# Kernel optimization log

Measured on AMD Instinct MI355X. Metric: run time of the kernel, lower is better.

Reference implementation:

```python
import jax, jax.numpy as jnp
import numpy as np
from jax import lax

B, C, H, W = 4, 3, 512, 512
PATCH = 64
STRIDE = 32
CHANS = [(3, 32), (32, 32), (32, 64), (64, 64), (64, 64), (64, 32), (32, 32), (32, 2)]


def _conv(x, w, b):
    y = lax.conv_general_dilated(x, w, (1, 1), [(1, 1), (1, 1)],
                                 dimension_numbers=('NCHW', 'OIHW', 'NCHW'))
    return y + b[None, :, None, None]


def _pool(x):  # MaxPool2d(2)
    return lax.reduce_window(x, -jnp.inf, lax.max, (1, 1, 2, 2), (1, 1, 2, 2), 'VALID')


def _up(x):  # Upsample(scale=2, bilinear, align_corners=False) == half-pixel resize
    b, c, h, w = x.shape
    return jax.image.resize(x, (b, c, 2 * h, 2 * w), 'bilinear')


def _flow_net(x, ws, bs):
    r = jax.nn.relu
    h = r(_conv(x, ws[0], bs[0]))
    h = r(_conv(h, ws[1], bs[1]))
    h = _pool(h)
    h = r(_conv(h, ws[2], bs[2]))
    h = r(_conv(h, ws[3], bs[3]))
    h = _pool(h)
    h = _up(h)
    h = r(_conv(h, ws[4], bs[4]))
    h = r(_conv(h, ws[5], bs[5]))
    h = _up(h)
    h = r(_conv(h, ws[6], bs[6]))
    return jnp.tanh(_conv(h, ws[7], bs[7]))  # [B,2,H,W]


def _bilinear_zeros(img, gx, gy):
    # img [C,H,W], gx/gy [N,P,P] in [-1,1]; grid_sample bilinear, zeros padding, align_corners=False
    Hh, Ww = img.shape[1], img.shape[2]
    ix = ((gx + 1.0) * Ww - 1.0) * 0.5
    iy = ((gy + 1.0) * Hh - 1.0) * 0.5
    x0 = jnp.floor(ix)
    y0 = jnp.floor(iy)
    wx1 = ix - x0
    wy1 = iy - y0

    def corner(xi, yi, wgt):
        valid = (xi >= 0) & (xi <= Ww - 1) & (yi >= 0) & (yi <= Hh - 1)
        xc = jnp.clip(xi, 0, Ww - 1).astype(jnp.int32)
        yc = jnp.clip(yi, 0, Hh - 1).astype(jnp.int32)
        return img[:, yc, xc] * (wgt * valid)[None]  # [C,N,P,P]

    return (corner(x0, y0, (1 - wx1) * (1 - wy1))
            + corner(x0 + 1, y0, wx1 * (1 - wy1))
            + corner(x0, y0 + 1, (1 - wx1) * wy1)
            + corner(x0 + 1, y0 + 1, wx1 * wy1))


def _forward(x, ws, bs, temp):
    b, c, h, w = x.shape
    flow = _flow_net(x, ws, bs)  # [B,2,H,W]
    gy, gx = jnp.meshgrid(jnp.linspace(-1.0, 1.0, h), jnp.linspace(-1.0, 1.0, w), indexing='ij')
    base = jnp.stack([gx, gy], axis=-1)  # [H,W,2] (x,y)
    deformed = base[None] + flow.transpose(0, 2, 3, 1) * temp  # [B,H,W,2]
    centers = deformed[:, ::STRIDE, ::STRIDE, :].reshape(b, -1, 2)  # [B,N,2]
    py, px = jnp.meshgrid(jnp.linspace(-1.0, 1.0, PATCH), jnp.linspace(-1.0, 1.0, PATCH), indexing='ij')
    pgx = centers[:, :, None, None, 0] + px[None, None] * (PATCH / w)  # [B,N,P,P]
    pgy = centers[:, :, None, None, 1] + py[None, None] * (PATCH / h)
    patches = jax.vmap(_bilinear_zeros)(x, pgx, pgy)  # [B,C,N,P,P]
    patches = patches.transpose(0, 2, 1, 3, 4)  # [B,N,C,P,P]
    return patches, flow, deformed


def setup_inputs() -> dict:
    key = jax.random.key(0)
    ks = jax.random.split(key, len(CHANS) + 1)
    d = {"x": jax.random.normal(ks[0], (B, C, H, W), jnp.float32)}
    for i, (ci, co) in enumerate(CHANS):
        d[f"w{i}"] = jax.random.normal(ks[i + 1], (co, ci, 3, 3), jnp.float32) * 0.01
        d[f"b{i}"] = jnp.zeros((co,), jnp.float32)
    d["temp"] = jnp.full((1,), 0.1, jnp.float32)
    return d


def reference(x, w0, b0, w1, b1, w2, b2, w3, b3, w4, b4, w5, b5, w6, b6, w7, b7, temp):
    ws = [w0, w1, w2, w3, w4, w5, w6, w7]
    bs = [b0, b1, b2, b3, b4, b5, b6, b7]
    return _forward(x, ws, bs, temp)
```

## Files before the change

### kernel.cpp

```cpp
#include <hip/hip_runtime.h>
#include <hip/hip_bf16.h>

typedef __hip_bfloat16 bf16;
typedef unsigned short ushort_t;
typedef __attribute__((ext_vector_type(8))) short short8;
typedef __attribute__((ext_vector_type(4))) float float4v;

#define BATCH 4
#define HH 512
#define WW 512

#define WO_L0 0
#define WO_L1 3072
#define WO_L2 12288
#define WO_L3 30720
#define WO_L4P 67584
#define WO_L5 215040
#define WO_L6P 233472
#define WO_L7 270336
#define WO_L4U 274944
#define WO_L6U 311808

__device__ __forceinline__ ushort_t f2bfu(float f) {
  __hip_bfloat16 h = __float2bfloat16(f);
// ... 24 lines not shown
  const int job = blockIdx.y;
  const int e = blockIdx.x * 256 + threadIdx.x;
  if (job == 0) {
    if (e >= 3072) return;
    int c = e & 7;
    int o = (e >> 3) & 31;
    int g = (e >> 8) % 3;
    int tl = (e >> 8) / 3;
    int tap = g * 4 + tl;
    float v = 0.0f;
    if (tap < 9 && c < 3) v = wp.w[0][(o * 3 + c) * 9 + tap];
    dst[WO_L0 + e] = __float2bfloat16(v);
    return;
  }
  if (job == 4 || job == 6) {
    const int O = (job == 4) ? 64 : 32;
    const int I = O;
    const int NCH = I >> 5;
    const int n = 4 * NCH * 9 * O * 32;
    if (e >= n) return;
    int ic = e & 31;
    int o = (e >> 5) % O;
    int tap = (e / (32 * O)) % 9;
    int ch = (e / (9 * 32 * O)) % NCH;
    int ph = e / (NCH * 9 * 32 * O);
    int i = ch * 32 + ic;
    int u = tap / 3, v2 = tap - u * 3;
    int dy = ph >> 1, dx = ph & 1;
    const float* w = wp.w[job];
    float acc = 0.0f;
#pragma unroll
    for (int r = 0; r < 3; ++r) {
      float ry = upw(r + dy, u);
#pragma unroll
      for (int s = 0; s < 3; ++s)
        acc += w[(o * I + i) * 9 + r * 3 + s] * ry * upw(s + dx, v2);
    }
    dst[((job == 4) ? WO_L4P : WO_L6P) + e] = __float2bfloat16(acc);
    return;
  }
  int O, I, OP, off;
  const float* w;
  if (job == 1)      { O = 32; I = 32; OP = 32; off = WO_L1; w = wp.w[1]; }
  else if (job == 2) { O = 64; I = 32; OP = 64; off = WO_L2; w = wp.w[2]; }
  else if (job == 3) { O = 64; I = 64; OP = 64; off = WO_L3; w = wp.w[3]; }
  else if (job == 5) { O = 32; I = 64; OP = 32; off = WO_L5; w = wp.w[5]; }
  else if (job == 7) { O = 2;  I = 32; OP = 16; off = WO_L7; w = wp.w[7]; }
  else if (job == 8) { O = 64; I = 64; OP = 64; off = WO_L4U; w = wp.w[4]; }
  else               { O = 32; I = 32; OP = 32; off = WO_L6U; w = wp.w[6]; }
  const int NCH = I >> 5;
  const int n = NCH * 9 * OP * 32;
  if (e >= n) return;
  int ic = e & 31;
  int o = (e >> 5) % OP;
  int tap = (e / (32 * OP)) % 9;
  int ch = e / (9 * 32 * OP);
  int i = ch * 32 + ic;
  float v = 0.0f;
  if (o < O) v = w[(o * I + i) * 9 + tap];
  dst[off + e] = __float2bfloat16(v);
}

__global__ __launch_bounds__(256) void pack_x(const float* __restrict__ x,
                                              bf16* __restrict__ xp) {
  int i = blockIdx.x * 256 + threadIdx.x;
  if (i >= BATCH * HH * WW) return;
  int b = i / (HH * WW);
  int px = i - b * (HH * WW);
  union { uint4 v; ushort_t s[8]; } o;
  o.v = make_uint4(0, 0, 0, 0);
  const float* p = x + (long)b * 3 * HH * WW + px;
  o.s[0] = f2bfu(p[0]);
  o.s[1] = f2bfu(p[HH * WW]);
  o.s[2] = f2bfu(p[2 * HH * WW]);
  *(uint4*)&xp[(long)i * 8] = o.v;
}

__global__ __launch_bounds__(512) void conv01_k(
    const bf16* __restrict__ xp, const bf16* __restrict__ w0,
    const bf16* __restrict__ w1, const float* __restrict__ b0,
    const float* __restrict__ b1, bf16* __restrict__ out) {
  __shared__ alignas(16) bf16 xp_lds[720 * 8];
  __shared__ alignas(16) bf16 mid_lds[612 * 32];
  __shared__ alignas(16) bf16 w0_lds[3072];
  __shared__ alignas(16) bf16 w1_lds[9 * 32 * 32];
  const int tid = threadIdx.x;
  const int lane = tid & 63;
  const int wid = tid >> 6;
  const int lm = lane & 15;
  const int quad = lane >> 4;
  const int x0 = blockIdx.x * 16, y0 = blockIdx.y * 32;
  const int b = blockIdx.z;

  for (int u = tid; u < 720; u += 512) {
    int hy = u / 20, hx = u - hy * 20;
    int gy = y0 - 2 + hy, gx = x0 - 2 + hx;
    uint4 v = make_uint4(0, 0, 0, 0);
    if (gy >= 0 && gy < HH && gx >= 0 && gx < WW)
      v = *(const uint4*)(xp + (((long)b * HH + gy) * WW + gx) * 8);
    *(uint4*)&xp_lds[u * 8] = v;
  }
  if (tid < 384) *(uint4*)&w0_lds[tid * 8] = *(const uint4*)(w0 + tid * 8);
  for (int j = wid; j < 18; j += 8)
    dma16((char*)w1_lds + j * 1024, (const char*)w1 + j * 1024 + lane * 16);
  __syncthreads();

  for (int t = wid; t < 39; t += 8) {
    int px = t * 16 + lm;
    int pxc = min(px, 611);
    int hy = pxc / 18, hx = pxc - hy * 18;
    float4v acc0[2];
#pragma unroll
    for (int mt = 0; mt < 2; ++mt)
      acc0[mt] = *(const float4v*)(b0 + mt * 16 + quad * 4);
#pragma unroll
    for (int g = 0; g < 3; ++g) {
      int tap = g * 4 + quad;
      if (tap > 8) tap = 8;
      int r = (tap * 11) >> 5;
      int s = tap - r * 3;
      short8 bfr = *(const short8*)&xp_lds[((hy + r) * 20 + hx + s) * 8];
      short8 a0 = *(const short8*)&w0_lds[quad * 768 + (g * 32 + lm) * 8];
      short8 a1 = *(const short8*)&w0_lds[quad * 768 + (g * 32 + 16 + lm) * 8];
      acc0[0] = __builtin_amdgcn_mfma_f32_16x16x32_bf16(a0, bfr, acc0[0], 0, 0, 0);
      acc0[1] = __builtin_amdgcn_mfma_f32_16x16x32_bf16(a1, bfr, acc0[1], 0, 0, 0);
    }
    int gy = y0 - 1 + hy, gx = x0 - 1 + hx;
    bool inimg = (gy >= 0) && (gy < HH) && (gx >= 0) && (gx < WW);
    if (px < 612) {
#pragma unroll
      for (int mt = 0; mt < 2; ++mt) {
        union { uint2 v; ushort_t s2[4]; } pk;
#pragma unroll
        for (int r2 = 0; r2 < 4; ++r2)
          pk.s2[r2] = inimg ? f2bfu(fmaxf(acc0[mt][r2], 0.0f)) : (ushort_t)0;
        *(uint2*)&mid_lds[px * 32 + mt * 16 + quad * 4] = pk.v;
      }
    }
  }
  __syncthreads();

  float4v acc[2][4];
#pragma unroll
  for (int mt = 0; mt < 2; ++mt) {
    float4v bv = *(const float4v*)(b1 + mt * 16 + quad * 4);
#pragma unroll
    for (int nt = 0; nt < 4; ++nt) acc[mt][nt] = bv;
  }
#pragma unroll
  for (int tap = 0; tap < 9; ++tap) {
    const int r = tap / 3, s = tap - r * 3;
    short8 afrag[2], bfrag[4];
#pragma unroll
    for (int mt = 0; mt < 2; ++mt)
      afrag[mt] = *(const short8*)&w1_lds[(tap * 32 + mt * 16 + lm) * 32 + quad * 8];
#pragma unroll
    for (int nt = 0; nt < 4; ++nt) {
      int py = 4 * wid + nt;
      bfrag[nt] = *(const short8*)&mid_lds[((py + r) * 18 + lm + s) * 32 + quad * 8];
    }
#pragma unroll
    for (int mt = 0; mt < 2; ++mt)
#pragma unroll
      for (int nt = 0; nt < 4; ++nt)
        acc[mt][nt] = __builtin_amdgcn_mfma_f32_16x16x32_bf16(
            afrag[mt], bfrag[nt], acc[mt][nt], 0, 0, 0);
  }
  const int Ho = HH >> 1, Wo = WW >> 1;
#pragma unroll
  for (int mt = 0; mt < 2; ++mt) {
#pragma unroll
    for (int g = 0; g < 2; ++g) {
      float4v m;
#pragma unroll
      for (int r = 0; r < 4; ++r)
        m[r] = fmaxf(fmaxf(acc[mt][2 * g][r], acc[mt][2 * g + 1][r]), 0.0f);
#pragma unroll
      for (int r = 0; r < 4; ++r) m[r] = fmaxf(m[r], __shfl_xor(m[r], 1, 64));
      if ((lm & 1) == 0) {
        int pyo = (y0 >> 1) + 2 * wid + g;
        int pxo = (x0 >> 1) + (lm >> 1);
        union { uint2 v; ushort_t s[4]; } pk;
#pragma unroll
        for (int r = 0; r < 4; ++r) pk.s[r] = f2bfu(m[r]);
        *(uint2*)&out[(((long)b * Ho + pyo) * Wo + pxo) * 32 + mt * 16 +
                      quad * 4] = pk.v;
      }
    }
  }
}

template <int CIN, int COUT, int COUTR, int OUT_MODE>
__global__ __launch_bounds__(512) void conv_mfma(
    const bf16* __restrict__ in, const bf16* __restrict__ wt,
    const float* __restrict__ bias, void* __restrict__ out_, int H, int W,
    const float* __restrict__ temp, float* __restrict__ def) {
  constexpr int MT = COUT / 16;
  constexpr int CK = 32;
  __shared__ alignas(16) bf16 in_lds[612 * CK];
  __shared__ alignas(16) bf16 w_lds[9 * COUT * CK];
  const int tid = threadIdx.x;
  const int lane = tid & 63;
  const int wid = tid >> 6;
  const int lm = lane & 15;
  const int quad = lane >> 4;
  const int x0 = blockIdx.x * 16;
  const int y0 = blockIdx.y * 32;
  const int b = blockIdx.z;

  float4v acc[MT][4];
#pragma unroll
  for (int mt = 0; mt < MT; ++mt) {
    float4v bv;
    if constexpr (COUTR == COUT) {
      bv = *(const float4v*)(bias + mt * 16 + quad * 4);
    } else {
#pragma unroll
      for (int r = 0; r < 4; ++r) {
        int co = mt * 16 + quad * 4 + r;
        bv[r] = (co < COUTR) ? bias[co] : 0.0f;
      }
    }
#pragma unroll
    for (int nt = 0; nt < 4; ++nt) acc[mt][nt] = bv;
  }

  const bool interior =
      (x0 >= 1) && (x0 + 16 <= W - 1) && (y0 >= 1) && (y0 + 32 <= H - 1);
  for (int c0 = 0; c0 < CIN; c0 += CK) {
    if (interior) {
      for (int r = wid; r < 34; r += 8) {
        int gy = y0 - 1 + r;
        const bf16* gsrc = in + (((long)b * H + gy) * W + x0) * CIN + c0 +
                           (lane >> 2) * CIN + (lane & 3) * 8;
        dma16(&in_lds[(r * 18 + 1) * CK], gsrc);
      }
      if (tid < 272) {
        int r = tid >> 3;
        int side = (tid >> 2) & 1;
        int seg = tid & 3;
        int gx = side ? (x0 + 16) : (x0 - 1);
        int gy = y0 - 1 + r;
        uint4 v = *(const uint4*)(in + (((long)b * H + gy) * W + gx) * CIN +
                                  c0 + seg * 8);
        *(uint4*)&in_lds[(r * 18 + (side ? 17 : 0)) * CK + seg * 8] = v;
      }
    } else {
      for (int u = tid; u < 612 * 4; u += 512) {
        int px = u >> 2;
        int seg = u & 3;
        int hy = px / 18, hx = px - hy * 18;
        int gy = y0 - 1 + hy, gx = x0 - 1 + hx;
        uint4 v = make_uint4(0, 0, 0, 0);
        if (gy >= 0 && gy < H && gx >= 0 && gx < W)
          v = *(const uint4*)(in + (((long)b * H + gy) * W + gx) * CIN + c0 +
                              seg * 8);
        *(uint4*)&in_lds[px * CK + seg * 8] = v;
      }
    }
    {
      const char* wsrc = (const char*)(wt + (size_t)(c0 >> 5) * 9 * COUT * CK);
      constexpr int WCH = 9 * COUT * CK * 2 / 1024;
      for (int j = wid; j < WCH; j += 8)
        dma16((char*)w_lds + j * 1024, wsrc + j * 1024 + lane * 16);
    }
    __syncthreads();

#pragma unroll
    for (int tap = 0; tap < 9; ++tap) {
      const int r = tap / 3, s = tap - r * 3;
      short8 afrag[MT], bfrag[4];
#pragma unroll
      for (int mt = 0; mt < MT; ++mt)
        afrag[mt] =
            *(const short8*)&w_lds[(tap * COUT + mt * 16 + lm) * CK + quad * 8];
#pragma unroll
      for (int nt = 0; nt < 4; ++nt) {
        int py = 4 * wid + nt;
        bfrag[nt] =
            *(const short8*)&in_lds[((py + r) * 18 + lm + s) * CK + quad * 8];
      }
#pragma unroll
      for (int mt = 0; mt < MT; ++mt)
#pragma unroll
        for (int nt = 0; nt < 4; ++nt)
          acc[mt][nt] = __builtin_amdgcn_mfma_f32_16x16x32_bf16(
              afrag[mt], bfrag[nt], acc[mt][nt], 0, 0, 0);
    }
    __syncthreads();
  }

  if constexpr (OUT_MODE == 3) {
    bf16* out = (bf16*)out_;
    const int Ho = H >> 1, Wo = W >> 1;
#pragma unroll
    for (int mt = 0; mt < MT; ++mt) {
#pragma unroll
      for (int g = 0; g < 2; ++g) {
        float4v m;
#pragma unroll
        for (int r = 0; r < 4; ++r)
          m[r] = fmaxf(fmaxf(acc[mt][2 * g][r], acc[mt][2 * g + 1][r]), 0.0f);
#pragma unroll
        for (int r = 0; r < 4; ++r) m[r] = fmaxf(m[r], __shfl_xor(m[r], 1, 64));
        if ((lm & 1) == 0) {
          int pyo = (y0 >> 1) + 2 * wid + g;
          int pxo = (x0 >> 1) + (lm >> 1);
          union { uint2 v; ushort_t s[4]; } pk;
#pragma unroll
          for (int r = 0; r < 4; ++r) pk.s[r] = f2bfu(m[r]);
          *(uint2*)&out[(((long)b * Ho + pyo) * Wo + pxo) * COUT + mt * 16 +
                        quad * 4] = pk.v;
        }
      }
    }
  } else {
#pragma unroll
    for (int mt = 0; mt < MT; ++mt) {
#pragma unroll
      for (int nt = 0; nt < 4; ++nt) {
        int gy = y0 + 4 * wid + nt;
        int gx = x0 + lm;
        float4v v = acc[mt][nt];
        if constexpr (OUT_MODE == 0) {
          bf16* out = (bf16*)out_;
          union { uint2 v; ushort_t s[4]; } pk;
#pragma unroll
          for (int r = 0; r < 4; ++r) pk.s[r] = f2bfu(fmaxf(v[r], 0.0f));
          *(uint2*)&out[(((long)b * H + gy) * W + gx) * COUT + mt * 16 +
                        quad * 4] = pk.v;
        } else {
          float* out = (float*)out_;
          if (quad == 0) {
            float fx = tanhf(v[0]);
            float fy = tanhf(v[1]);
            out[(((long)b * 2 + 0) * H + gy) * (long)W + gx] = fx;
            out[(((long)b * 2 + 1) * H + gy) * (long)W + gx] = fy;
            float T = temp[0];
            float2 d;
            d.x = -1.0f + gx * (2.0f / 511.0f) + fx * T;
            d.y = -1.0f + gy * (2.0f / 511.0f) + fy * T;
            *(float2*)&def[(((long)b * HH + gy) * WW + gx) * 2] = d;
          }
        }
      }
    }
  }
}

template <int CIN, int COUT, bool PSPLIT>
__global__ __launch_bounds__(512) void conv_up(
    const bf16* __restrict__ in, const bf16* __restrict__ wtP,
    const bf16* __restrict__ wtU, const float* __restrict__ bias,
    bf16* __restrict__ out, int Ho, int Wo) {
  constexpr int MT = COUT / 16;
  constexpr int MH = MT / 2;
  constexpr int CK = 32;
  constexpr int WSZ = 9 * COUT * CK;
  constexpr int WBUF = PSPLIT ? WSZ : 2 * WSZ;
  __shared__ alignas(16) bf16 in_lds[612 * CK];
  __shared__ alignas(16) bf16 w_lds[WBUF];
  const int tid = threadIdx.x;
  const int lane = tid & 63;
  const int wid = tid >> 6;
  const int lm = lane & 15;
  const int quad = lane >> 4;
  const int Hs = Ho >> 1, Ws = Wo >> 1;
  const int nx = Ws >> 4, ny = Hs >> 5;
  const int bulkN = nx * ny;
  const int b = PSPLIT ? (blockIdx.z >> 2) : blockIdx.z;
  const int ph0 = PSPLIT ? (blockIdx.z & 3) : 0;
  const int t = blockIdx.x;

  if (t >= bulkN) {
    if (PSPLIT && ph0 != 0) return;
    const int G = Wo >> 4;
    int e = t - bulkN;
    int tx, ty;
    if (e < G) { ty = 0; tx = e; }
    else if (e < 2 * G) { ty = G - 1; tx = e - G; }
    else { int u = e - 2 * G; ty = 1 + (u >> 1); tx = (u & 1) ? (G - 1) : 0; }
    const int x0 = tx * 16, y0 = ty * 16;
    const int wrow = wid & 3;
    const int wmt = (wid >> 2) * MH;

    float4v acc[MH][4];
#pragma unroll
    for (int m = 0; m < MH; ++m) {
      float4v bv = *(const float4v*)(bias + (wmt + m) * 16 + quad * 4);
#pragma unroll
      for (int nt = 0; nt < 4; ++nt) acc[m][nt] = bv;
    }

    for (int c0 = 0; c0 < CIN; c0 += CK) {
      for (int u = tid; u < 324 * 4; u += 512) {
        int px = u >> 2;
        int seg = u & 3;
        int hy = px / 18, hx = px - hy * 18;
        int gy = y0 - 1 + hy, gx = x0 - 1 + hx;
        uint4 o = make_uint4(0, 0, 0, 0);
        if (gy >= 0 && gy < Ho && gx >= 0 && gx < Wo) {
          int ys = (gy >> 1) - ((gy & 1) ? 0 : 1);
          int xs = (gx >> 1) - ((gx & 1) ? 0 : 1);
          float wy = (gy & 1) ? 0.25f : 0.75f;
          float wx = (gx & 1) ? 0.25f : 0.75f;
          int y0c = max(ys, 0), y1c = min(ys + 1, Hs - 1);
          int x0c = max(xs, 0), x1c = min(xs + 1, Ws - 1);
          const bf16* p = in + ((long)b * Hs * Ws) * CIN + c0 + seg * 8;
          union { uint4 v; ushort_t s[8]; } a00, a01, a10, a11, r;
          a00.v = *(const uint4*)(p + ((long)y0c * Ws + x0c) * CIN);
          a01.v = *(const uint4*)(p + ((long)y0c * Ws + x1c) * CIN);
          a10.v = *(const uint4*)(p + ((long)y1c * Ws + x0c) * CIN);
          a11.v = *(const uint4*)(p + ((long)y1c * Ws + x1c) * CIN);
#pragma unroll
          for (int j = 0; j < 8; ++j) {
            float f = (1.0f - wy) * ((1.0f - wx) * bfu2f(a00.s[j]) +
                                     wx * bfu2f(a01.s[j])) +
                      wy * ((1.0f - wx) * bfu2f(a10.s[j]) +
                            wx * bfu2f(a11.s[j]));
            r.s[j] = f2bfu(f);
          }
          o = r.v;
        }
        *(uint4*)&in_lds[px * CK + seg * 8] = o;
      }
      {
        const char* wsrc = (const char*)(wtU + (size_t)(c0 >> 5) * WSZ);
        constexpr int WCH = WSZ * 2 / 1024;
        for (int j = wid; j < WCH; j += 8)
          dma16((char*)w_lds + j * 1024, wsrc + j * 1024 + lane * 16);
      }
      __syncthreads();
#pragma unroll
      for (int tap = 0; tap < 9; ++tap) {
        const int r = tap / 3, s = tap - r * 3;
        short8 afrag[MH], bfrag[4];
#pragma unroll
        for (int m = 0; m < MH; ++m)
          afrag[m] = *(const short8*)&w_lds[(tap * COUT + (wmt + m) * 16 + lm) * CK +
                                            quad * 8];
#pragma unroll
        for (int nt = 0; nt < 4; ++nt) {
          int py = 4 * wrow + nt;
          bfrag[nt] =
              *(const short8*)&in_lds[((py + r) * 18 + lm + s) * CK + quad * 8];
        }
#pragma unroll
        for (int m = 0; m < MH; ++m)
#pragma unroll
          for (int nt = 0; nt < 4; ++nt)
            acc[m][nt] = __builtin_amdgcn_mfma_f32_16x16x32_bf16(
                afrag[m], bfrag[nt], acc[m][nt], 0, 0, 0);
      }
      __syncthreads();
    }
#pragma unroll
    for (int m = 0; m < MH; ++m)
#pragma unroll
      for (int nt = 0; nt < 4; ++nt) {
        int gy = y0 + 4 * wrow + nt;
        int gx = x0 + lm;
        union { uint2 v; ushort_t s[4]; } pk;
#pragma unroll
        for (int r = 0; r < 4; ++r) pk.s[r] = f2bfu(fmaxf(acc[m][nt][r], 0.0f));
        *(uint2*)&out[(((long)b * Ho + gy) * Wo + gx) * COUT + (wmt + m) * 16 +
                      quad * 4] = pk.v;
      }
    return;
  }

  const int bx = t % nx, by = t / nx;
  const int xs0 = bx * 16, ys0 = by * 32;
  const bool interior = (bx >= 1) && (bx < nx - 1) && (by >= 1) && (by < ny - 1);

  if constexpr (!PSPLIT) {
    static_assert(CIN == CK, "non-split bulk path assumes single K chunk");
    if (interior) {
      for (int r = wid; r < 34; r += 8) {
        int gy = ys0 - 1 + r;
        const bf16* gsrc = in + (((long)b * Hs + gy) * Ws + xs0) * CIN +
                           (lane >> 2) * CIN + (lane & 3) * 8;
        dma16(&in_lds[(r * 18 + 1) * CK], gsrc);
      }
      if (tid < 272) {
        int r = tid >> 3;
        int side = (tid >> 2) & 1;
        int seg = tid & 3;
        int gx = side ? (xs0 + 16) : (xs0 - 1);
        int gy = ys0 - 1 + r;
        uint4 v = *(const uint4*)(in + (((long)b * Hs + gy) * Ws + gx) * CIN +
                                  seg * 8);
        *(uint4*)&in_lds[(r * 18 + (side ? 17 : 0)) * CK + seg * 8] = v;
      }
    } else {
      for (int u = tid; u < 612 * 4; u += 512) {
        int px = u >> 2;
        int seg = u & 3;
        int hy = px / 18, hx = px - hy * 18;
        int sy = min(max(ys0 - 1 + hy, 0), Hs - 1);
        int sx = min(max(xs0 - 1 + hx, 0), Ws - 1);
        uint4 v = *(const uint4*)(in + (((long)b * Hs + sy) * Ws + sx) * CIN +
                                  seg * 8);
        *(uint4*)&in_lds[px * CK + seg * 8] = v;
      }
    }
    constexpr int WCH = 2 * WSZ * 2 / 1024;
    for (int pair = 0; pair < 2; ++pair) {
      {
        const char* wsrc = (const char*)(wtP + (size_t)(2 * pair) * WSZ);
        for (int j = wid; j < WCH; j += 8)
          dma16((char*)w_lds + j * 1024, wsrc + j * 1024 + lane * 16);
      }
      __syncthreads();
      float4v acc[2][MT][4];
#pragma unroll
      for (int p = 0; p < 2; ++p)
#pragma unroll
        for (int mt = 0; mt < MT; ++mt) {
          float4v bv = *(const float4v*)(bias + mt * 16 + quad * 4);
#pragma unroll
          for (int nt = 0; nt < 4; ++nt) acc[p][mt][nt] = bv;
        }
#pragma unroll
      for (int tap = 0; tap < 9; ++tap) {
        const int r = tap / 3, s = tap - r * 3;
        short8 bfrag[4], afrag[2][MT];
#pragma unroll
        for (int nt = 0; nt < 4; ++nt) {
          int py = 4 * wid + nt;
          bfrag[nt] =
              *(const short8*)&in_lds[((py + r) * 18 + lm + s) * CK + quad * 8];
        }
#pragma unroll
        for (int p = 0; p < 2; ++p)
#pragma unroll
          for (int mt = 0; mt < MT; ++mt)
            afrag[p][mt] = *(const short8*)&w_lds[p * WSZ +
                (tap * COUT + mt * 16 + lm) * CK + quad * 8];
#pragma unroll
        for (int p = 0; p < 2; ++p)
#pragma unroll
          for (int mt = 0; mt < MT; ++mt)
#pragma unroll
            for (int nt = 0; nt < 4; ++nt)
              acc[p][mt][nt] = __builtin_amdgcn_mfma_f32_16x16x32_bf16(
                  afrag[p][mt], bfrag[nt], acc[p][mt][nt], 0, 0, 0);
      }
      const int dy = pair;
#pragma unroll
      for (int p = 0; p < 2; ++p) {
        const int dx = p;
#pragma unroll
        for (int mt = 0; mt < MT; ++mt)
#pragma unroll
          for (int nt = 0; nt < 4; ++nt) {
            int gy = 2 * (ys0 + 4 * wid + nt) + dy;
            int gx = 2 * (xs0 + lm) + dx;
            if (gy >= 16 && gy < Ho - 16 && gx >= 16 && gx < Wo - 16) {
              union { uint2 v; ushort_t s2[4]; } pk;
#pragma unroll
              for (int r2 = 0; r2 < 4; ++r2)
                pk.s2[r2] = f2bfu(fmaxf(acc[p][mt][nt][r2], 0.0f));
              *(uint2*)&out[(((long)b * Ho + gy) * Wo + gx) * COUT + mt * 16 +
                            quad * 4] = pk.v;
            }
          }
      }
      __syncthreads();
    }
    return;
  }

  const int ph = ph0;
  float4v acc[MT][4];
#pragma unroll
  for (int mt = 0; mt < MT; ++mt) {
    float4v bv = *(const float4v*)(bias + mt * 16 + quad * 4);
#pragma unroll
    for (int nt = 0; nt < 4; ++nt) acc[mt][nt] = bv;
  }
  for (int c0 = 0; c0 < CIN; c0 += CK) {
    if (interior) {
      for (int r = wid; r < 34; r += 8) {
        int gy = ys0 - 1 + r;
        const bf16* gsrc = in + (((long)b * Hs + gy) * Ws + xs0) * CIN +
                           c0 + (lane >> 2) * CIN + (lane & 3) * 8;
        dma16(&in_lds[(r * 18 + 1) * CK], gsrc);
      }
      if (tid < 272) {
        int r = tid >> 3;
        int side = (tid >> 2) & 1;
        int seg = tid & 3;
        int gx = side ? (xs0 + 16) : (xs0 - 1);
        int gy = ys0 - 1 + r;
        uint4 v = *(const uint4*)(in + (((long)b * Hs + gy) * Ws + gx) * CIN +
                                  c0 + seg * 8);
        *(uint4*)&in_lds[(r * 18 + (side ? 17 : 0)) * CK + seg * 8] = v;
      }
    } else {
      for (int u = tid; u < 612 * 4; u += 512) {
        int px = u >> 2;
        int seg = u & 3;
        int hy = px / 18, hx = px - hy * 18;
        int sy = min(max(ys0 - 1 + hy, 0), Hs - 1);
        int sx = min(max(xs0 - 1 + hx, 0), Ws - 1);
        uint4 v = *(const uint4*)(in + (((long)b * Hs + sy) * Ws + sx) * CIN +
                                  seg * 8);
        *(uint4*)&in_lds[px * CK + seg * 8] = v;
      }
    }
    {
      const char* wsrc = (const char*)(wtP + (size_t)(ph * (CIN / CK) + (c0 >> 5)) * WSZ);
      constexpr int WCH = WSZ * 2 / 1024;
      for (int j = wid; j < WCH; j += 8)
        dma16((char*)w_lds + j * 1024, wsrc + j * 1024 + lane * 16);
    }
    __syncthreads();
#pragma unroll
    for (int tap = 0; tap < 9; ++tap) {
      const int r = tap / 3, s = tap - r * 3;
      short8 afrag[MT], bfrag[4];
#pragma unroll
      for (int mt = 0; mt < MT; ++mt)
        afrag[mt] =
            *(const short8*)&w_lds[(tap * COUT + mt * 16 + lm) * CK + quad * 8];
#pragma unroll
      for (int nt = 0; nt < 4; ++nt) {
        int py = 4 * wid + nt;
        bfrag[nt] =
            *(const short8*)&in_lds[((py + r) * 18 + lm + s) * CK + quad * 8];
      }
#pragma unroll
      for (int mt = 0; mt < MT; ++mt)
#pragma unroll
        for (int nt = 0; nt < 4; ++nt)
          acc[mt][nt] = __builtin_amdgcn_mfma_f32_16x16x32_bf16(
              afrag[mt], bfrag[nt], acc[mt][nt], 0, 0, 0);
    }
    __syncthreads();
  }
  const int dy = ph >> 1, dx = ph & 1;
#pragma unroll
  for (int mt = 0; mt < MT; ++mt)
#pragma unroll
    for (int nt = 0; nt < 4; ++nt) {
      int gy = 2 * (ys0 + 4 * wid + nt) + dy;
      int gx = 2 * (xs0 + lm) + dx;
      if (gy >= 16 && gy < Ho - 16 && gx >= 16 && gx < Wo - 16) {
        union { uint2 v; ushort_t s2[4]; } pk;
#pragma unroll
        for (int r2 = 0; r2 < 4; ++r2)
          pk.s2[r2] = f2bfu(fmaxf(acc[mt][nt][r2], 0.0f));
        *(uint2*)&out[(((long)b * Ho + gy) * Wo + gx) * COUT + mt * 16 +
                      quad * 4] = pk.v;
      }
    }
}

__global__ __launch_bounds__(256) void patches_k(const float* __restrict__ x,
                                                 const float* __restrict__ def,
                                                 float* __restrict__ out) {
  int i = blockIdx.x * 256 + threadIdx.x;
  int pj = i & 63;
  int t = i >> 6;
  int pi = t & 63;
  t >>= 6;
  int n = t & 255;
  int b = t >> 8;
  if (b >= BATCH) return;
  int hi = n >> 4, wi = n & 15;
  const float* dptr = def + (((long)b * HH + hi * 32) * WW + wi * 32) * 2;
  float cx = dptr[0], cy = dptr[1];
  float pgx = cx + (-1.0f + pj * (2.0f / 63.0f)) * 0.125f;
  float pgy = cy + (-1.0f + pi * (2.0f / 63.0f)) * 0.125f;
  float ix = ((pgx + 1.0f) * 512.0f - 1.0f) * 0.5f;
  float iy = ((pgy + 1.0f) * 512.0f - 1.0f) * 0.5f;
  float fx0 = floorf(ix), fy0 = floorf(iy);
  float wx1 = ix - fx0, wy1 = iy - fy0;
  int x0 = (int)fx0, y0 = (int)fy0;
  int x1 = x0 + 1, y1 = y0 + 1;
  bool vx0 = (x0 >= 0) && (x0 <= 511), vx1 = (x1 >= 0) && (x1 <= 511);
  bool vy0 = (y0 >= 0) && (y0 <= 511), vy1 = (y1 >= 0) && (y1 <= 511);
  int cx0 = min(max(x0, 0), 511), cx1 = min(max(x1, 0), 511);
  int cy0 = min(max(y0, 0), 511), cy1 = min(max(y1, 0), 511);
  float w00 = (1.0f - wx1) * (1.0f - wy1) * ((vx0 && vy0) ? 1.0f : 0.0f);
  float w01 = wx1 * (1.0f - wy1) * ((vx1 && vy0) ? 1.0f : 0.0f);
  float w10 = (1.0f - wx1) * wy1 * ((vx0 && vy1) ? 1.0f : 0.0f);
  float w11 = wx1 * wy1 * ((vx1 && vy1) ? 1.0f : 0.0f);
#pragma unroll
  for (int c = 0; c < 3; ++c) {
    const float* img = x + ((long)b * 3 + c) * (HH * WW);
    float v = img[cy0 * WW + cx0] * w00 + img[cy0 * WW + cx1] * w01 +
              img[cy1 * WW + cx0] * w10 + img[cy1 * WW + cx1] * w11;
    out[(((long)b * 256 + n) * 3 + c) * 4096 + pi * 64 + pj] = v;
  }
}


extern "C" void kernel_launch(void* const* d_in, const int* in_sizes, int n_in,
                              void* d_out, int out_size, void* d_ws,
                              size_t ws_size, hipStream_t stream) {
  const float* x = (const float*)d_in[0];
  WP wp;
  const float* bs[8];
  for (int i = 0; i < 8; ++i) {
    wp.w[i] = (const float*)d_in[1 + 2 * i];
    bs[i] = (const float*)d_in[2 + 2 * i];
  }
  const float* temp = (const float*)d_in[17];

  float* out = (float*)d_out;
  float* flow = out + 12582912;
  float* def = out + 14680064;
  bf16* wT = (bf16*)d_out;

  const size_t bufElems = (size_t)BATCH * 512 * 512 * 32;
  bf16* A = (bf16*)d_ws;
  bf16* Bf = A + bufElems;
  bf16* xp = Bf + bufElems;

  prep_w<<<dim3(576, 10), 256, 0, stream>>>(wp, wT);
  pack_x<<<(BATCH * HH * WW) / 256, 256, 0, stream>>>(x, xp);
// ... 18 lines not shown
```

Baseline: 317.5 us.

## Read conv weight fragments directly from global memory instead of staging in LDS

Removes the LDS weight buffers from all conv kernels and loads the MFMA A-fragments straight from global memory, relying on L1/L2 caching of the small weight tensors. This drops the per-chunk weight DMA and cuts LDS usage, which may allow more blocks per CU, and it reorders barriers so only one sync sits between chunk iterations. The cost is more global and cache traffic inside the MFMA inner loop, which adds latency there. It also fixes a missing c0 offset in the edge-tile load path of the upsampled conv.

```diff
diff --git a/kernel.cpp b/kernel.cpp
--- a/kernel.cpp
+++ b/kernel.cpp
@@ -130,8 +130,6 @@
     const float* __restrict__ b1, bf16* __restrict__ out) {
   __shared__ alignas(16) bf16 xp_lds[720 * 8];
   __shared__ alignas(16) bf16 mid_lds[612 * 32];
-  __shared__ alignas(16) bf16 w0_lds[3072];
-  __shared__ alignas(16) bf16 w1_lds[9 * 32 * 32];
   const int tid = threadIdx.x;
   const int lane = tid & 63;
   const int wid = tid >> 6;
@@ -148,9 +146,6 @@
       v = *(const uint4*)(xp + (((long)b * HH + gy) * WW + gx) * 8);
     *(uint4*)&xp_lds[u * 8] = v;
   }
-  if (tid < 384) *(uint4*)&w0_lds[tid * 8] = *(const uint4*)(w0 + tid * 8);
-  for (int j = wid; j < 18; j += 8)
-    dma16((char*)w1_lds + j * 1024, (const char*)w1 + j * 1024 + lane * 16);
   __syncthreads();
 
   for (int t = wid; t < 39; t += 8) {
@@ -168,8 +163,8 @@
       int r = (tap * 11) >> 5;
       int s = tap - r * 3;
       short8 bfr = *(const short8*)&xp_lds[((hy + r) * 20 + hx + s) * 8];
-      short8 a0 = *(const short8*)&w0_lds[quad * 768 + (g * 32 + lm) * 8];
-      short8 a1 = *(const short8*)&w0_lds[quad * 768 + (g * 32 + 16 + lm) * 8];
+      short8 a0 = *(const short8*)&w0[quad * 768 + (g * 32 + lm) * 8];
+      short8 a1 = *(const short8*)&w0[quad * 768 + (g * 32 + 16 + lm) * 8];
       acc0[0] = __builtin_amdgcn_mfma_f32_16x16x32_bf16(a0, bfr, acc0[0], 0, 0, 0);
       acc0[1] = __builtin_amdgcn_mfma_f32_16x16x32_bf16(a1, bfr, acc0[1], 0, 0, 0);
     }
@@ -201,7 +196,7 @@
     short8 afrag[2], bfrag[4];
 #pragma unroll
     for (int mt = 0; mt < 2; ++mt)
-      afrag[mt] = *(const short8*)&w1_lds[(tap * 32 + mt * 16 + lm) * 32 + quad * 8];
+      afrag[mt] = *(const short8*)&w1[(tap * 32 + mt * 16 + lm) * 32 + quad * 8];
 #pragma unroll
     for (int nt = 0; nt < 4; ++nt) {
       int py = 4 * wid + nt;
@@ -246,7 +241,6 @@
   constexpr int MT = COUT / 16;
   constexpr int CK = 32;
   __shared__ alignas(16) bf16 in_lds[612 * CK];
-  __shared__ alignas(16) bf16 w_lds[9 * COUT * CK];
   const int tid = threadIdx.x;
   const int lane = tid & 63;
   const int wid = tid >> 6;
@@ -276,6 +270,7 @@
   const bool interior =
       (x0 >= 1) && (x0 + 16 <= W - 1) && (y0 >= 1) && (y0 + 32 <= H - 1);
   for (int c0 = 0; c0 < CIN; c0 += CK) {
+    if (c0) __syncthreads();
     if (interior) {
       for (int r = wid; r < 34; r += 8) {
         int gy = y0 - 1 + r;
@@ -306,14 +301,9 @@
         *(uint4*)&in_lds[px * CK + seg * 8] = v;
       }
     }
-    {
-      const char* wsrc = (const char*)(wt + (size_t)(c0 >> 5) * 9 * COUT * CK);
-      constexpr int WCH = 9 * COUT * CK * 2 / 1024;
-      for (int j = wid; j < WCH; j += 8)
-        dma16((char*)w_lds + j * 1024, wsrc + j * 1024 + lane * 16);
-    }
     __syncthreads();
 
+    const bf16* wc = wt + (size_t)(c0 >> 5) * 9 * COUT * CK;
 #pragma unroll
     for (int tap = 0; tap < 9; ++tap) {
       const int r = tap / 3, s = tap - r * 3;
@@ -321,7 +311,7 @@
 #pragma unroll
       for (int mt = 0; mt < MT; ++mt)
         afrag[mt] =
-            *(const short8*)&w_lds[(tap * COUT + mt * 16 + lm) * CK + quad * 8];
+            *(const short8*)&wc[(tap * COUT + mt * 16 + lm) * CK + quad * 8];
 #pragma unroll
       for (int nt = 0; nt < 4; ++nt) {
         int py = 4 * wid + nt;
@@ -335,7 +325,6 @@
           acc[mt][nt] = __builtin_amdgcn_mfma_f32_16x16x32_bf16(
               afrag[mt], bfrag[nt], acc[mt][nt], 0, 0, 0);
     }
-    __syncthreads();
   }
 
   if constexpr (OUT_MODE == 3) {
@@ -405,9 +394,7 @@
   constexpr int MH = MT / 2;
   constexpr int CK = 32;
   constexpr int WSZ = 9 * COUT * CK;
-  constexpr int WBUF = PSPLIT ? WSZ : 2 * WSZ;
   __shared__ alignas(16) bf16 in_lds[612 * CK];
-  __shared__ alignas(16) bf16 w_lds[WBUF];
   const int tid = threadIdx.x;
   const int lane = tid & 63;
   const int wid = tid >> 6;
@@ -441,6 +428,7 @@
     }
 
     for (int c0 = 0; c0 < CIN; c0 += CK) {
+      if (c0) __syncthreads();
       for (int u = tid; u < 324 * 4; u += 512) {
         int px = u >> 2;
         int seg = u & 3;
@@ -472,21 +460,16 @@
         }
         *(uint4*)&in_lds[px * CK + seg * 8] = o;
       }
-      {
-        const char* wsrc = (const char*)(wtU + (size_t)(c0 >> 5) * WSZ);
-        constexpr int WCH = WSZ * 2 / 1024;
-        for (int j = wid; j < WCH; j += 8)
-          dma16((char*)w_lds + j * 1024, wsrc + j * 1024 + lane * 16);
-      }
       __syncthreads();
+      const bf16* wc = wtU + (size_t)(c0 >> 5) * WSZ;
 #pragma unroll
       for (int tap = 0; tap < 9; ++tap) {
         const int r = tap / 3, s = tap - r * 3;
         short8 afrag[MH], bfrag[4];
 #pragma unroll
         for (int m = 0; m < MH; ++m)
-          afrag[m] = *(const short8*)&w_lds[(tap * COUT + (wmt + m) * 16 + lm) * CK +
-                                            quad * 8];
+          afrag[m] = *(const short8*)&wc[(tap * COUT + (wmt + m) * 16 + lm) * CK +
+                                         quad * 8];
 #pragma unroll
         for (int nt = 0; nt < 4; ++nt) {
           int py = 4 * wrow + nt;
@@ -500,7 +483,6 @@
             acc[m][nt] = __builtin_amdgcn_mfma_f32_16x16x32_bf16(
                 afrag[m], bfrag[nt], acc[m][nt], 0, 0, 0);
       }
-      __syncthreads();
     }
 #pragma unroll
     for (int m = 0; m < MH; ++m)
@@ -552,14 +534,9 @@
         *(uint4*)&in_lds[px * CK + seg * 8] = v;
       }
     }
-    constexpr int WCH = 2 * WSZ * 2 / 1024;
+    __syncthreads();
+
     for (int pair = 0; pair < 2; ++pair) {
-      {
-        const char* wsrc = (const char*)(wtP + (size_t)(2 * pair) * WSZ);
-        for (int j = wid; j < WCH; j += 8)
-          dma16((char*)w_lds + j * 1024, wsrc + j * 1024 + lane * 16);
-      }
-      __syncthreads();
       float4v acc[2][MT][4];
 #pragma unroll
       for (int p = 0; p < 2; ++p)
@@ -569,6 +546,7 @@
 #pragma unroll
           for (int nt = 0; nt < 4; ++nt) acc[p][mt][nt] = bv;
         }
+      const bf16* w0p = wtP + (size_t)(2 * pair) * WSZ;
 #pragma unroll
       for (int tap = 0; tap < 9; ++tap) {
         const int r = tap / 3, s = tap - r * 3;
@@ -583,7 +561,7 @@
         for (int p = 0; p < 2; ++p)
 #pragma unroll
           for (int mt = 0; mt < MT; ++mt)
-            afrag[p][mt] = *(const short8*)&w_lds[p * WSZ +
+            afrag[p][mt] = *(const short8*)&w0p[(size_t)p * WSZ +
                 (tap * COUT + mt * 16 + lm) * CK + quad * 8];
 #pragma unroll
         for (int p = 0; p < 2; ++p)
@@ -614,7 +592,6 @@
             }
           }
       }
-      __syncthreads();
     }
     return;
   }
@@ -628,6 +605,7 @@
     for (int nt = 0; nt < 4; ++nt) acc[mt][nt] = bv;
   }
   for (int c0 = 0; c0 < CIN; c0 += CK) {
+    if (c0) __syncthreads();
     if (interior) {
       for (int r = wid; r < 34; r += 8) {
         int gy = ys0 - 1 + r;
@@ -653,17 +631,12 @@
         int sy = min(max(ys0 - 1 + hy, 0), Hs - 1);
         int sx = min(max(xs0 - 1 + hx, 0), Ws - 1);
         uint4 v = *(const uint4*)(in + (((long)b * Hs + sy) * Ws + sx) * CIN +
-                                  seg * 8);
+                                  c0 + seg * 8);
         *(uint4*)&in_lds[px * CK + seg * 8] = v;
       }
     }
-    {
-      const char* wsrc = (const char*)(wtP + (size_t)(ph * (CIN / CK) + (c0 >> 5)) * WSZ);
-      constexpr int WCH = WSZ * 2 / 1024;
-      for (int j = wid; j < WCH; j += 8)
-        dma16((char*)w_lds + j * 1024, wsrc + j * 1024 + lane * 16);
-    }
     __syncthreads();
+    const bf16* wc = wtP + (size_t)(ph * (CIN / CK) + (c0 >> 5)) * WSZ;
 #pragma unroll
     for (int tap = 0; tap < 9; ++tap) {
       const int r = tap / 3, s = tap - r * 3;
@@ -671,7 +644,7 @@
 #pragma unroll
       for (int mt = 0; mt < MT; ++mt)
         afrag[mt] =
-            *(const short8*)&w_lds[(tap * COUT + mt * 16 + lm) * CK + quad * 8];
+            *(const short8*)&wc[(tap * COUT + mt * 16 + lm) * CK + quad * 8];
 #pragma unroll
       for (int nt = 0; nt < 4; ++nt) {
         int py = 4 * wid + nt;
@@ -685,7 +658,6 @@
           acc[mt][nt] = __builtin_amdgcn_mfma_f32_16x16x32_bf16(
               afrag[mt], bfrag[nt], acc[mt][nt], 0, 0, 0);
     }
-    __syncthreads();
   }
   const int dy = ph >> 1, dx = ph & 1;
 #pragma unroll
```

New measurement: 359.6 us. +13.3%, slower.

## Stage conv weights in LDS one kernel row at a time to cut LDS footprint

Applied to the files above, without the earlier changes.

The weight tile in shared memory now holds only 3 taps (one kernel row) instead of all 9, in both conv_mfma and conv_up. Each input-channel chunk now runs three load/sync/compute rounds that reuse the same input halo. The aim is to free LDS so more blocks fit on each CU. The cost is three times as many barriers and weight loads that are exposed rather than overlapped. The clamped border path of the phase-split branch also now adds the missing c0 channel offset, which fixes a correctness bug when CIN is greater than 32.

```diff
diff --git a/kernel.cpp b/kernel.cpp
--- a/kernel.cpp
+++ b/kernel.cpp
@@ -246,7 +246,7 @@
   constexpr int MT = COUT / 16;
   constexpr int CK = 32;
   __shared__ alignas(16) bf16 in_lds[612 * CK];
-  __shared__ alignas(16) bf16 w_lds[9 * COUT * CK];
+  __shared__ alignas(16) bf16 w_lds[3 * COUT * CK];
   const int tid = threadIdx.x;
   const int lane = tid & 63;
   const int wid = tid >> 6;
@@ -276,66 +276,71 @@
   const bool interior =
       (x0 >= 1) && (x0 + 16 <= W - 1) && (y0 >= 1) && (y0 + 32 <= H - 1);
   for (int c0 = 0; c0 < CIN; c0 += CK) {
-    if (interior) {
-      for (int r = wid; r < 34; r += 8) {
-        int gy = y0 - 1 + r;
-        const bf16* gsrc = in + (((long)b * H + gy) * W + x0) * CIN + c0 +
-                           (lane >> 2) * CIN + (lane & 3) * 8;
-        dma16(&in_lds[(r * 18 + 1) * CK], gsrc);
-      }
-      if (tid < 272) {
-        int r = tid >> 3;
-        int side = (tid >> 2) & 1;
-        int seg = tid & 3;
-        int gx = side ? (x0 + 16) : (x0 - 1);
-        int gy = y0 - 1 + r;
-        uint4 v = *(const uint4*)(in + (((long)b * H + gy) * W + gx) * CIN +
+    for (int tg = 0; tg < 3; ++tg) {
+      if (tg == 0) {
+        if (interior) {
+          for (int r = wid; r < 34; r += 8) {
+            int gy = y0 - 1 + r;
+            const bf16* gsrc = in + (((long)b * H + gy) * W + x0) * CIN + c0 +
+                               (lane >> 2) * CIN + (lane & 3) * 8;
+            dma16(&in_lds[(r * 18 + 1) * CK], gsrc);
+          }
+          if (tid < 272) {
+            int r = tid >> 3;
+            int side = (tid >> 2) & 1;
+            int seg = tid & 3;
+            int gx = side ? (x0 + 16) : (x0 - 1);
+            int gy = y0 - 1 + r;
+            uint4 v = *(const uint4*)(in + (((long)b * H + gy) * W + gx) * CIN +
+                                      c0 + seg * 8);
+            *(uint4*)&in_lds[(r * 18 + (side ? 17 : 0)) * CK + seg * 8] = v;
+          }
+        } else {
+          for (int u = tid; u < 612 * 4; u += 512) {
+            int px = u >> 2;
+            int seg = u & 3;
+            int hy = px / 18, hx = px - hy * 18;
+            int gy = y0 - 1 + hy, gx = x0 - 1 + hx;
+            uint4 v = make_uint4(0, 0, 0, 0);
+            if (gy >= 0 && gy < H && gx >= 0 && gx < W)
+              v = *(const uint4*)(in + (((long)b * H + gy) * W + gx) * CIN +
                                   c0 + seg * 8);
-        *(uint4*)&in_lds[(r * 18 + (side ? 17 : 0)) * CK + seg * 8] = v;
-      }
-    } else {
-      for (int u = tid; u < 612 * 4; u += 512) {
-        int px = u >> 2;
-        int seg = u & 3;
-        int hy = px / 18, hx = px - hy * 18;
-        int gy = y0 - 1 + hy, gx = x0 - 1 + hx;
-        uint4 v = make_uint4(0, 0, 0, 0);
-        if (gy >= 0 && gy < H && gx >= 0 && gx < W)
-          v = *(const uint4*)(in + (((long)b * H + gy) * W + gx) * CIN + c0 +
-                              seg * 8);
-        *(uint4*)&in_lds[px * CK + seg * 8] = v;
-      }
-    }
-    {
-      const char* wsrc = (const char*)(wt + (size_t)(c0 >> 5) * 9 * COUT * CK);
-      constexpr int WCH = 9 * COUT * CK * 2 / 1024;
-      for (int j = wid; j < WCH; j += 8)
-        dma16((char*)w_lds + j * 1024, wsrc + j * 1024 + lane * 16);
-    }
-    __syncthreads();
-
-#pragma unroll
-    for (int tap = 0; tap < 9; ++tap) {
-      const int r = tap / 3, s = tap - r * 3;
-      short8 afrag[MT], bfrag[4];
-#pragma unroll
-      for (int mt = 0; mt < MT; ++mt)
-        afrag[mt] =
-            *(const short8*)&w_lds[(tap * COUT + mt * 16 + lm) * CK + quad * 8];
-#pragma unroll
-      for (int nt = 0; nt < 4; ++nt) {
-        int py = 4 * wid + nt;
-        bfrag[nt] =
-            *(const short8*)&in_lds[((py + r) * 18 + lm + s) * CK + quad * 8];
-      }
-#pragma unroll
-      for (int mt = 0; mt < MT; ++mt)
-#pragma unroll
-        for (int nt = 0; nt < 4; ++nt)
-          acc[mt][nt] = __builtin_amdgcn_mfma_f32_16x16x32_bf16(
-              afrag[mt], bfrag[nt], acc[mt][nt], 0, 0, 0);
-    }
-    __syncthreads();
+            *(uint4*)&in_lds[px * CK + seg * 8] = v;
+          }
+        }
+      }
+      {
+        const char* wsrc =
+            (const char*)(wt + ((size_t)(c0 >> 5) * 9 + 3 * tg) * COUT * CK);
+        constexpr int WCH = 3 * COUT * CK * 2 / 1024;
+        for (int j = wid; j < WCH; j += 8)
+          dma16((char*)w_lds + j * 1024, wsrc + j * 1024 + lane * 16);
+      }
+      __syncthreads();
+
+#pragma unroll
+      for (int t3 = 0; t3 < 3; ++t3) {
+        const int r = tg, s = t3;
+        short8 afrag[MT], bfrag[4];
+#pragma unroll
+        for (int mt = 0; mt < MT; ++mt)
+          afrag[mt] =
+              *(const short8*)&w_lds[(t3 * COUT + mt * 16 + lm) * CK + quad * 8];
+#pragma unroll
+        for (int nt = 0; nt < 4; ++nt) {
+          int py = 4 * wid + nt;
+          bfrag[nt] =
+              *(const short8*)&in_lds[((py + r) * 18 + lm + s) * CK + quad * 8];
+        }
+#pragma unroll
+        for (int mt = 0; mt < MT; ++mt)
+#pragma unroll
+          for (int nt = 0; nt < 4; ++nt)
+            acc[mt][nt] = __builtin_amdgcn_mfma_f32_16x16x32_bf16(
+                afrag[mt], bfrag[nt], acc[mt][nt], 0, 0, 0);
+      }
+      __syncthreads();
+    }
   }
 
   if constexpr (OUT_MODE == 3) {
@@ -405,9 +410,10 @@
   constexpr int MH = MT / 2;
   constexpr int CK = 32;
   constexpr int WSZ = 9 * COUT * CK;
-  constexpr int WBUF = PSPLIT ? WSZ : 2 * WSZ;
+  constexpr int WROW = 3 * COUT * CK;
+  constexpr int NWB = PSPLIT ? 1 : 2;
   __shared__ alignas(16) bf16 in_lds[612 * CK];
-  __shared__ alignas(16) bf16 w_lds[WBUF];
+  __shared__ alignas(16) bf16 w_lds[NWB * WROW];
   const int tid = threadIdx.x;
   const int lane = tid & 63;
   const int wid = tid >> 6;
@@ -441,66 +447,71 @@
     }
 
     for (int c0 = 0; c0 < CIN; c0 += CK) {
-      for (int u = tid; u < 324 * 4; u += 512) {
-        int px = u >> 2;
-        int seg = u & 3;
-        int hy = px / 18, hx = px - hy * 18;
-        int gy = y0 - 1 + hy, gx = x0 - 1 + hx;
-        uint4 o = make_uint4(0, 0, 0, 0);
-        if (gy >= 0 && gy < Ho && gx >= 0 && gx < Wo) {
-          int ys = (gy >> 1) - ((gy & 1) ? 0 : 1);
-          int xs = (gx >> 1) - ((gx & 1) ? 0 : 1);
-          float wy = (gy & 1) ? 0.25f : 0.75f;
-          float wx = (gx & 1) ? 0.25f : 0.75f;
-          int y0c = max(ys, 0), y1c = min(ys + 1, Hs - 1);
-          int x0c = max(xs, 0), x1c = min(xs + 1, Ws - 1);
-          const bf16* p = in + ((long)b * Hs * Ws) * CIN + c0 + seg * 8;
-          union { uint4 v; ushort_t s[8]; } a00, a01, a10, a11, r;
-          a00.v = *(const uint4*)(p + ((long)y0c * Ws + x0c) * CIN);
-          a01.v = *(const uint4*)(p + ((long)y0c * Ws + x1c) * CIN);
-          a10.v = *(const uint4*)(p + ((long)y1c * Ws + x0c) * CIN);
-          a11.v = *(const uint4*)(p + ((long)y1c * Ws + x1c) * CIN);
-#pragma unroll
-          for (int j = 0; j < 8; ++j) {
-            float f = (1.0f - wy) * ((1.0f - wx) * bfu2f(a00.s[j]) +
-                                     wx * bfu2f(a01.s[j])) +
-                      wy * ((1.0f - wx) * bfu2f(a10.s[j]) +
-                            wx * bfu2f(a11.s[j]));
-            r.s[j] = f2bfu(f);
-          }
-          o = r.v;
-        }
-        *(uint4*)&in_lds[px * CK + seg * 8] = o;
-      }
-      {
-        const char* wsrc = (const char*)(wtU + (size_t)(c0 >> 5) * WSZ);
-        constexpr int WCH = WSZ * 2 / 1024;
-        for (int j = wid; j < WCH; j += 8)
-          dma16((char*)w_lds + j * 1024, wsrc + j * 1024 + lane * 16);
-      }
-      __syncthreads();
-#pragma unroll
-      for (int tap = 0; tap < 9; ++tap) {
-        const int r = tap / 3, s = tap - r * 3;
-        short8 afrag[MH], bfrag[4];
-#pragma unroll
-        for (int m = 0; m < MH; ++m)
-          afrag[m] = *(const short8*)&w_lds[(tap * COUT + (wmt + m) * 16 + lm) * CK +
-                                            quad * 8];
-#pragma unroll
-        for (int nt = 0; nt < 4; ++nt) {
-          int py = 4 * wrow + nt;
-          bfrag[nt] =
-              *(const short8*)&in_lds[((py + r) * 18 + lm + s) * CK + quad * 8];
-        }
-#pragma unroll
-        for (int m = 0; m < MH; ++m)
-#pragma unroll
-          for (int nt = 0; nt < 4; ++nt)
-            acc[m][nt] = __builtin_amdgcn_mfma_f32_16x16x32_bf16(
-                afrag[m], bfrag[nt], acc[m][nt], 0, 0, 0);
-      }
-      __syncthreads();
+      for (int tg = 0; tg < 3; ++tg) {
+        if (tg == 0) {
+          for (int u = tid; u < 324 * 4; u += 512) {
+            int px = u >> 2;
+            int seg = u & 3;
+            int hy = px / 18, hx = px - hy * 18;
+            int gy = y0 - 1 + hy, gx = x0 - 1 + hx;
+            uint4 o = make_uint4(0, 0, 0, 0);
+            if (gy >= 0 && gy < Ho && gx >= 0 && gx < Wo) {
+              int ys = (gy >> 1) - ((gy & 1) ? 0 : 1);
+              int xs = (gx >> 1) - ((gx & 1) ? 0 : 1);
+              float wy = (gy & 1) ? 0.25f : 0.75f;
+              float wx = (gx & 1) ? 0.25f : 0.75f;
+              int y0c = max(ys, 0), y1c = min(ys + 1, Hs - 1);
+              int x0c = max(xs, 0), x1c = min(xs + 1, Ws - 1);
+              const bf16* p = in + ((long)b * Hs * Ws) * CIN + c0 + seg * 8;
+              union { uint4 v; ushort_t s[8]; } a00, a01, a10, a11, r;
+              a00.v = *(const uint4*)(p + ((long)y0c * Ws + x0c) * CIN);
+              a01.v = *(const uint4*)(p + ((long)y0c * Ws + x1c) * CIN);
+              a10.v = *(const uint4*)(p + ((long)y1c * Ws + x0c) * CIN);
+              a11.v = *(const uint4*)(p + ((long)y1c * Ws + x1c) * CIN);
+#pragma unroll
+              for (int j = 0; j < 8; ++j) {
+                float f = (1.0f - wy) * ((1.0f - wx) * bfu2f(a00.s[j]) +
+                                         wx * bfu2f(a01.s[j])) +
+                          wy * ((1.0f - wx) * bfu2f(a10.s[j]) +
+                                wx * bfu2f(a11.s[j]));
+                r.s[j] = f2bfu(f);
+              }
+              o = r.v;
+            }
+            *(uint4*)&in_lds[px * CK + seg * 8] = o;
+          }
+        }
+        {
+          const char* wsrc =
+              (const char*)(wtU + ((size_t)(c0 >> 5) * 9 + 3 * tg) * COUT * CK);
+          constexpr int WCH = 3 * COUT * CK * 2 / 1024;
+          for (int j = wid; j < WCH; j += 8)
+            dma16((char*)w_lds + j * 1024, wsrc + j * 1024 + lane * 16);
+        }
+        __syncthreads();
+#pragma unroll
+        for (int t3 = 0; t3 < 3; ++t3) {
+          const int r = tg, s = t3;
+          short8 afrag[MH], bfrag[4];
+#pragma unroll
+          for (int m = 0; m < MH; ++m)
+            afrag[m] = *(const short8*)&w_lds[(t3 * COUT + (wmt + m) * 16 + lm) *
+                                                  CK + quad * 8];
+#pragma unroll
+          for (int nt = 0; nt < 4; ++nt) {
+            int py = 4 * wrow + nt;
+            bfrag[nt] =
+                *(const short8*)&in_lds[((py + r) * 18 + lm + s) * CK + quad * 8];
+          }
+#pragma unroll
+          for (int m = 0; m < MH; ++m)
+#pragma unroll
+            for (int nt = 0; nt < 4; ++nt)
+              acc[m][nt] = __builtin_amdgcn_mfma_f32_16x16x32_bf16(
+                  afrag[m], bfrag[nt], acc[m][nt], 0, 0, 0);
+        }
+        __syncthreads();
+      }
     }
 #pragma unroll
     for (int m = 0; m < MH; ++m)
@@ -552,14 +563,8 @@
         *(uint4*)&in_lds[px * CK + seg * 8] = v;
       }
     }
-    constexpr int WCH = 2 * WSZ * 2 / 1024;
+
     for (int pair = 0; pair < 2; ++pair) {
-      {
-        const char* wsrc = (const char*)(wtP + (size_t)(2 * pair) * WSZ);
-        for (int j = wid; j < WCH; j += 8)
-          dma16((char*)w_lds + j * 1024, wsrc + j * 1024 + lane * 16);
-      }
-      __syncthreads();
       float4v acc[2][MT][4];
 #pragma unroll
       for (int p = 0; p < 2; ++p)
@@ -569,30 +574,43 @@
 #pragma unroll
           for (int nt = 0; nt < 4; ++nt) acc[p][mt][nt] = bv;
         }
-#pragma unroll
-      for (int tap = 0; tap < 9; ++tap) {
-        const int r = tap / 3, s = tap - r * 3;
-        short8 bfrag[4], afrag[2][MT];
-#pragma unroll
-        for (int nt = 0; nt < 4; ++nt) {
-          int py = 4 * wid + nt;
-          bfrag[nt] =
-              *(const short8*)&in_lds[((py + r) * 18 + lm + s) * CK + quad * 8];
-        }
-#pragma unroll
-        for (int p = 0; p < 2; ++p)
-#pragma unroll
-          for (int mt = 0; mt < MT; ++mt)
-            afrag[p][mt] = *(const short8*)&w_lds[p * WSZ +
-                (tap * COUT + mt * 16 + lm) * CK + quad * 8];
-#pragma unroll
-        for (int p = 0; p < 2; ++p)
-#pragma unroll
-          for (int mt = 0; mt < MT; ++mt)
-#pragma unroll
-            for (int nt = 0; nt < 4; ++nt)
-              acc[p][mt][nt] = __builtin_amdgcn_mfma_f32_16x16x32_bf16(
-                  afrag[p][mt], bfrag[nt], acc[p][mt][nt], 0, 0, 0);
+      for (int tg = 0; tg < 3; ++tg) {
+        {
+          constexpr int WCH1 = 3 * COUT * CK * 2 / 1024;
+          for (int j = wid; j < 2 * WCH1; j += 8) {
+            int p = j / WCH1, jj = j - p * WCH1;
+            const char* wsrc = (const char*)(wtP +
+                ((size_t)(2 * pair + p) * 9 + 3 * tg) * COUT * CK);
+            dma16((char*)w_lds + j * 1024, wsrc + jj * 1024 + lane * 16);
+          }
+        }
+        __syncthreads();
+#pragma unroll
+        for (int t3 = 0; t3 < 3; ++t3) {
+          const int r = tg, s = t3;
+          short8 bfrag[4], afrag[2][MT];
+#pragma unroll
+          for (int nt = 0; nt < 4; ++nt) {
+            int py = 4 * wid + nt;
+            bfrag[nt] =
+                *(const short8*)&in_lds[((py + r) * 18 + lm + s) * CK + quad * 8];
+          }
+#pragma unroll
+          for (int p = 0; p < 2; ++p)
+#pragma unroll
+            for (int mt = 0; mt < MT; ++mt)
+              afrag[p][mt] = *(const short8*)&w_lds[p * WROW +
+                  (t3 * COUT + mt * 16 + lm) * CK + quad * 8];
+#pragma unroll
+          for (int p = 0; p < 2; ++p)
+#pragma unroll
+            for (int mt = 0; mt < MT; ++mt)
+#pragma unroll
+              for (int nt = 0; nt < 4; ++nt)
+                acc[p][mt][nt] = __builtin_amdgcn_mfma_f32_16x16x32_bf16(
+                    afrag[p][mt], bfrag[nt], acc[p][mt][nt], 0, 0, 0);
+        }
+        __syncthreads();
       }
       const int dy = pair;
 #pragma unroll
@@ -614,7 +632,6 @@
             }
           }
       }
-      __syncthreads();
     }
     return;
   }
@@ -628,64 +645,69 @@
     for (int nt = 0; nt < 4; ++nt) acc[mt][nt] = bv;
   }
   for (int c0 = 0; c0 < CIN; c0 += CK) {
-    if (interior) {
-      for (int r = wid; r < 34; r += 8) {
-        int gy = ys0 - 1 + r;
-        const bf16* gsrc = in + (((long)b * Hs + gy) * Ws + xs0) * CIN +
-                           c0 + (lane >> 2) * CIN + (lane & 3) * 8;
-        dma16(&in_lds[(r * 18 + 1) * CK], gsrc);
-      }
-      if (tid < 272) {
-        int r = tid >> 3;
-        int side = (tid >> 2) & 1;
-        int seg = tid & 3;
-        int gx = side ? (xs0 + 16) : (xs0 - 1);
-        int gy = ys0 - 1 + r;
-        uint4 v = *(const uint4*)(in + (((long)b * Hs + gy) * Ws + gx) * CIN +
-                                  c0 + seg * 8);
-        *(uint4*)&in_lds[(r * 18 + (side ? 17 : 0)) * CK + seg * 8] = v;
-      }
-    } else {
-      for (int u = tid; u < 612 * 4; u += 512) {
-        int px = u >> 2;
-        int seg = u & 3;
-        int hy = px / 18, hx = px - hy * 18;
-        int sy = min(max(ys0 - 1 + hy, 0), Hs - 1);
-        int sx = min(max(xs0 - 1 + hx, 0), Ws - 1);
-        uint4 v = *(const uint4*)(in + (((long)b * Hs + sy) * Ws + sx) * CIN +
-                                  seg * 8);
-        *(uint4*)&in_lds[px * CK + seg * 8] = v;
-      }
-    }
-    {
-      const char* wsrc = (const char*)(wtP + (size_t)(ph * (CIN / CK) + (c0 >> 5)) * WSZ);
-      constexpr int WCH = WSZ * 2 / 1024;
-      for (int j = wid; j < WCH; j += 8)
-        dma16((char*)w_lds + j * 1024, wsrc + j * 1024 + lane * 16);
-    }
-    __syncthreads();
-#pragma unroll
-    for (int tap = 0; tap < 9; ++tap) {
-      const int r = tap / 3, s = tap - r * 3;
-      short8 afrag[MT], bfrag[4];
-#pragma unroll
-      for (int mt = 0; mt < MT; ++mt)
-        afrag[mt] =
-            *(const short8*)&w_lds[(tap * COUT + mt * 16 + lm) * CK + quad * 8];
-#pragma unroll
-      for (int nt = 0; nt < 4; ++nt) {
-        int py = 4 * wid + nt;
-        bfrag[nt] =
-            *(const short8*)&in_lds[((py + r) * 18 + lm + s) * CK + quad * 8];
-      }
-#pragma unroll
-      for (int mt = 0; mt < MT; ++mt)
-#pragma unroll
-        for (int nt = 0; nt < 4; ++nt)
-          acc[mt][nt] = __builtin_amdgcn_mfma_f32_16x16x32_bf16(
-              afrag[mt], bfrag[nt], acc[mt][nt], 0, 0, 0);
-    }
-    __syncthreads();
+    for (int tg = 0; tg < 3; ++tg) {
+      if (tg == 0) {
+        if (interior) {
+          for (int r = wid; r < 34; r += 8) {
+            int gy = ys0 - 1 + r;
+            const bf16* gsrc = in + (((long)b * Hs + gy) * Ws + xs0) * CIN +
+                               c0 + (lane >> 2) * CIN + (lane & 3) * 8;
+            dma16(&in_lds[(r * 18 + 1) * CK], gsrc);
+          }
+          if (tid < 272) {
+            int r = tid >> 3;
+            int side = (tid >> 2) & 1;
+            int seg = tid & 3;
+            int gx = side ? (xs0 + 16) : (xs0 - 1);
+            int gy = ys0 - 1 + r;
+            uint4 v = *(const uint4*)(in + (((long)b * Hs + gy) * Ws + gx) * CIN +
+                                      c0 + seg * 8);
+            *(uint4*)&in_lds[(r * 18 + (side ? 17 : 0)) * CK + seg * 8] = v;
+          }
+        } else {
+          for (int u = tid; u < 612 * 4; u += 512) {
+            int px = u >> 2;
+            int seg = u & 3;
+            int hy = px / 18, hx = px - hy * 18;
+            int sy = min(max(ys0 - 1 + hy, 0), Hs - 1);
+            int sx = min(max(xs0 - 1 + hx, 0), Ws - 1);
+            uint4 v = *(const uint4*)(in + (((long)b * Hs + sy) * Ws + sx) * CIN +
+                                      c0 + seg * 8);
+            *(uint4*)&in_lds[px * CK + seg * 8] = v;
+          }
+        }
+      }
+      {
+        const char* wsrc = (const char*)(wtP +
+            ((size_t)(ph * (CIN / CK) + (c0 >> 5)) * 9 + 3 * tg) * COUT * CK);
+        constexpr int WCH = 3 * COUT * CK * 2 / 1024;
+        for (int j = wid; j < WCH; j += 8)
+          dma16((char*)w_lds + j * 1024, wsrc + j * 1024 + lane * 16);
+      }
+      __syncthreads();
+#pragma unroll
+      for (int t3 = 0; t3 < 3; ++t3) {
+        const int r = tg, s = t3;
+        short8 afrag[MT], bfrag[4];
+#pragma unroll
+        for (int mt = 0; mt < MT; ++mt)
+          afrag[mt] =
+              *(const short8*)&w_lds[(t3 * COUT + mt * 16 + lm) * CK + quad * 8];
+#pragma unroll
+        for (int nt = 0; nt < 4; ++nt) {
+          int py = 4 * wid + nt;
+          bfrag[nt] =
+              *(const short8*)&in_lds[((py + r) * 18 + lm + s) * CK + quad * 8];
+        }
+#pragma unroll
+        for (int mt = 0; mt < MT; ++mt)
+#pragma unroll
+          for (int nt = 0; nt < 4; ++nt)
+            acc[mt][nt] = __builtin_amdgcn_mfma_f32_16x16x32_bf16(
+                afrag[mt], bfrag[nt], acc[mt][nt], 0, 0, 0);
+      }
+      __syncthreads();
+    }
   }
   const int dy = ph >> 1, dx = ph & 1;
 #pragma unroll
```

Result: slower. 336.9 us (+6.1%).
